# Kernel tuning notes

Measured on AMD Instinct MI355X. Metric: run time of the kernel, lower is better.

The kernel has to match this reference:

```python
import jax, jax.numpy as jnp
import numpy as np
from jax.ops import segment_sum, segment_min, segment_max

N, E = 25000, 400000
NF, EF = 30, 10
H = 40          # n_hidden (multiple of towers)
T = 5           # towers
F = H           # F_in per tower (divide_input=False)
FO = H // T     # F_out per tower
L = 2           # gnn layers
NC = 2          # classes
EPS_BN = 1e-5


def setup_inputs() -> dict:
    key = jax.random.key(0)
    ks = jax.random.split(key, 24)
    r = lambda k, s, sc=0.1: jax.random.normal(k, s, jnp.float32) * sc
    return {
        "x": jax.random.normal(ks[0], (N, NF), jnp.float32),
        "edge_attr": jax.random.normal(ks[1], (E, EF), jnp.float32),
        "edge_index": jax.random.randint(ks[2], (2, E), 0, N, jnp.int32),
        "node_w": r(ks[3], (NF, H)), "node_b": r(ks[4], (H,)),
        "edge_w": r(ks[5], (EF, H)), "edge_b": r(ks[6], (H,)),
        "enc_w": r(ks[7], (L, H, F)), "enc_b": r(ks[8], (L, F)),
        "pre_w": r(ks[9], (L, T, 3 * F, F)), "pre_b": r(ks[10], (L, T, F)),
        "post_w": r(ks[11], (L, T, 13 * F, FO)), "post_b": r(ks[12], (L, T, FO)),
        "lin_w": r(ks[13], (L, H, H)), "lin_b": r(ks[14], (L, H)),
        "bn_g": jnp.ones((L, H), jnp.float32), "bn_b": jnp.zeros((L, H), jnp.float32),
        "mlp1_w": r(ks[15], (3 * H, 50)), "mlp1_b": r(ks[16], (50,)),
        "mlp2_w": r(ks[17], (50, 25)), "mlp2_b": r(ks[18], (25,)),
        "mlp3_w": r(ks[19], (25, NC)), "mlp3_b": r(ks[20], (NC,)),
    }


def _pna_conv(x, src, dst, e_emb, enc_w, enc_b, pre_w, pre_b, post_w, post_b,
              lin_w, lin_b, cnt, cnt1, amp, att):
    # message: per-tower pre-MLP on cat(x_i=dst, x_j=src, enc(edge_attr))
    e = e_emb @ enc_w + enc_b                                    # [E, F]
    h = jnp.concatenate([x[dst], x[src], e], axis=-1)            # [E, 3F]
    hs = jnp.einsum('ef,tfo->eto', h, pre_w) + pre_b             # [E, T, F]
    # multi-aggregation over incoming edges (index = dst)
    c = cnt1[:, None, None]
    mean = segment_sum(hs, dst, num_segments=N) / c
    msq = segment_sum(hs * hs, dst, num_segments=N) / c
    std = jnp.sqrt(jax.nn.relu(msq - mean * mean) + 1e-5)
    has = (cnt > 0)[:, None, None]
    mn = jnp.where(has, segment_min(hs, dst, num_segments=N), 0.0)
    mx = jnp.where(has, segment_max(hs, dst, num_segments=N), 0.0)
    agg = jnp.concatenate([mean, mn, mx, std], axis=-1)          # [N, T, 4F]
    agg = jnp.concatenate([agg, agg * amp, agg * att], axis=-1)  # [N, T, 12F]
    out = jnp.concatenate(
        [jnp.broadcast_to(x[:, None, :], (N, T, F)), agg], axis=-1)  # [N, T, 13F]
    out = jnp.einsum('ntf,tfo->nto', out, post_w) + post_b       # [N, T, FO]
    return out.reshape(N, T * FO) @ lin_w + lin_b                # [N, H]


def reference(x, edge_attr, node_w, node_b, edge_w, edge_b, enc_w, enc_b,
              pre_w, pre_b, post_w, post_b, lin_w, lin_b, bn_g, bn_b,
              mlp1_w, mlp1_b, mlp2_w, mlp2_b, mlp3_w, mlp3_b, edge_index):
    src, dst = edge_index[0], edge_index[1]
    cnt = segment_sum(jnp.ones((E,), jnp.float32), dst, num_segments=N)  # in-degree
    cnt1 = jnp.maximum(cnt, 1.0)                                 # deg.clamp_(1)
    log_deg = jnp.log(cnt1 + 1.0)
    avg_log = jnp.mean(jnp.log(cnt + 1.0))                       # PNA avg_deg['log']
    amp = (log_deg / avg_log)[:, None, None]
    att = (avg_log / log_deg)[:, None, None]
    h = x @ node_w + node_b                                      # node embedding
    e_emb = edge_attr @ edge_w + edge_b                          # edge embedding
    for i in range(L):
        c = _pna_conv(h, src, dst, e_emb, enc_w[i], enc_b[i], pre_w[i], pre_b[i],
                      post_w[i], post_b[i], lin_w[i], lin_b[i], cnt, cnt1, amp, att)
        mu = jnp.mean(c, axis=0)
        var = jnp.mean((c - mu) ** 2, axis=0)                    # BatchNorm (batch stats)
        cbn = (c - mu) / jnp.sqrt(var + EPS_BN) * bn_g[i] + bn_b[i]
        h = (h + jax.nn.relu(cbn)) / 2.0
    z = jax.nn.relu(jnp.concatenate([h[src], h[dst]], axis=-1))  # [E, 2H]
    z = jnp.concatenate([z, e_emb], axis=-1)                     # [E, 3H]
    z = jax.nn.relu(z @ mlp1_w + mlp1_b)
    z = jax.nn.relu(z @ mlp2_w + mlp2_b)
    return z @ mlp3_w + mlp3_b                                   # [E, NC]
```

## Files before the change

### kernel.cpp

```cpp
#include <hip/hip_runtime.h>
#include <hip/hip_bf16.h>
#include <cstdint>
#include <cstddef>

#define NN 25000
#define NE 400000
#define NFD 30
#define EFD 10
#define H 40
#define T 5
#define FO 8
#define LAYERS 2
#define TF 200
#define BASE_W 800
#define PSTR 52
#define WS_PAD 532
#define REC 12
#define WCN 416
#define WCK 64
#define SHP 72
#define EPSV 1e-5f

typedef __attribute__((ext_vector_type(8))) short bf16x8;
typedef __attribute__((ext_vector_type(4))) float f32x4;

__device__ inline short bfbits(float v) {
    __hip_bfloat16 b = __float2bfloat16(v);
    return *(short*)&b;
}

__global__ __launch_bounds__(256) void k_deg(const int* __restrict__ dst, int* __restrict__ cnt) {
    int e = blockIdx.x * 256 + threadIdx.x;
    if (e < NE) atomicAdd(&cnt[dst[e]], 1);
}

__global__ __launch_bounds__(256) void k_avglog(const int* __restrict__ cnt, float* __restrict__ slot) {
    __shared__ float red[256];
    float s = 0.0f;
    for (int i = blockIdx.x * 256 + threadIdx.x; i < NN; i += gridDim.x * 256)
        s += logf((float)cnt[i] + 1.0f);
    red[threadIdx.x] = s; __syncthreads();
    for (int o = 128; o > 0; o >>= 1) {
        if (threadIdx.x < o) red[threadIdx.x] += red[threadIdx.x + o];
        __syncthreads();
    }
    if (threadIdx.x == 0) atomicAdd(slot, red[0]);
}

__global__ __launch_bounds__(256) void k_node(const float* __restrict__ x, const float* __restrict__ w,
                                              const float* __restrict__ b, float* __restrict__ h,
                                              const int* __restrict__ cnt, const float* __restrict__ slot,
                                              float* __restrict__ amp, float* __restrict__ att) {
    int id = blockIdx.x * 256 + threadIdx.x;
    if (id < NN) {
        float avg = slot[0] / (float)NN;
        float c1 = fmaxf((float)cnt[id], 1.0f);
        float lg = logf(c1 + 1.0f);
        amp[id] = lg / avg;
        att[id] = avg / lg;
    }
    if (id >= NN * H) return;
    int n = id / H, j = id - n * H;
    const float* xr = x + (size_t)n * NFD;
    float acc = b[j];
    #pragma unroll
    for (int m = 0; m < NFD; m++) acc += xr[m] * w[m * H + j];
    h[id] = acc;
}

__global__ __launch_bounds__(1024) void k_scan(const int* __restrict__ cnt, int* __restrict__ offs) {
    __shared__ int wsum[16];
    int tid = threadIdx.x;
    int lane = tid & 63, wv = tid >> 6;
    int runbase = 0;
    for (int base = 0; base < NN; base += 4096) {
        int i0 = base + tid * 4;
        int4 v = make_int4(0, 0, 0, 0);
        if (i0 < NN) v = *(const int4*)(cnt + i0);
        int tsum = v.x + v.y + v.z + v.w;
        int x = tsum;
        #pragma unroll
        for (int o = 1; o < 64; o <<= 1) {
            int y = __shfl_up(x, o);
            if (lane >= o) x += y;
        }
        if (lane == 63) wsum[wv] = x;
        __syncthreads();
        if (wv == 0 && lane < 16) {
            int wsv = wsum[lane];
            #pragma unroll
            for (int o = 1; o < 16; o <<= 1) {
                int y = __shfl_up(wsv, o);
                if (lane >= o) wsv += y;
            }
            wsum[lane] = wsv;
        }
        __syncthreads();
        int wpref = (wv > 0) ? wsum[wv - 1] : 0;
        int excl = runbase + wpref + x - tsum;
        if (i0 < NN) {
            offs[i0]     = excl;
            offs[i0 + 1] = excl + v.x;
            offs[i0 + 2] = excl + v.x + v.y;
            offs[i0 + 3] = excl + v.x + v.y + v.z;
        }
        runbase += wsum[15];
        __syncthreads();
    }
    if (tid == 0) offs[NN] = runbase;
}

__global__ __launch_bounds__(256) void k_scatter(const int* __restrict__ src, const int* __restrict__ dst,
                                                 const float* __restrict__ edge_attr,
                                                 const int* __restrict__ offs, int* __restrict__ fill,
                                                 float* __restrict__ ea_csr, int* __restrict__ pdst) {
    int e = blockIdx.x * 256 + threadIdx.x;
    if (e >= NE) return;
    int d = dst[e];
    int p = offs[d] + atomicAdd(&fill[d], 1);
    const float2* ear = (const float2*)(edge_attr + (size_t)e * EFD);
    float2 v0 = ear[0], v1 = ear[1], v2 = ear[2], v3 = ear[3], v4 = ear[4];
    float4* o = (float4*)(ea_csr + (size_t)p * REC);
    o[0] = make_float4(v0.x, v0.y, v1.x, v1.y);
    o[1] = make_float4(v2.x, v2.y, v3.x, v3.y);
    o[2] = make_float4(v4.x, v4.y, __int_as_float(src[e]), __int_as_float(e));
    pdst[p] = d;
}

__global__ __launch_bounds__(256) void k_prep1(const float* __restrict__ enc_w, const float* __restrict__ enc_b,
                                               const float* __restrict__ edge_w, const float* __restrict__ edge_b,
                                               const float* __restrict__ pre_w, const float* __restrict__ pre_b,
                                               const float* __restrict__ w1, const float* __restrict__ b1,
                                               float* __restrict__ W3e, float* __restrict__ dvecF,
                                               __hip_bfloat16* __restrict__ Wcat,
                                               float* __restrict__ W1e, float* __restrict__ b1e, int layer) {
    int id = blockIdx.x * 256 + threadIdx.x;
    if (id < EFD * TF) {
        int m = id / TF, j = id - m * TF;
        int t = j / H, f = j - t * H;
        const float* ew = enc_w + (size_t)layer * H * H;
        const float* pw = pre_w + (size_t)(layer * T + t) * 120 * H;
        float acc = 0.0f;
        for (int k = 0; k < H; k++) {
            float wk = edge_w[m * H + k];
            float g = 0.0f;
            #pragma unroll
            for (int o = 0; o < H; o++) g += ew[k * H + o] * pw[(80 + o) * H + f];
            acc += wk * g;
        }
        W3e[m * TF + j] = acc;
        if (m == 0) {
            const float* eb = enc_b + (size_t)layer * H;
            float dacc = pre_b[(size_t)(layer * T + t) * H + f];
            for (int o = 0; o < H; o++) {
                float ebe = eb[o];
                #pragma unroll
                for (int k = 0; k < H; k++) ebe += edge_b[k] * ew[k * H + o];
                dacc += ebe * pw[(80 + o) * H + f];
            }
            dvecF[j] = dacc;
        }
    } else if (id < EFD * TF + WCN * WCK) {
        int id2 = id - EFD * TF;
        int j = id2 / WCK, k = id2 - j * WCK;
        float val = 0.0f;
        if (k < H) {
            if (j < TF) {
                int t = j / H, f = j - t * H;
                val = pre_w[((size_t)(layer * T + t) * 120 + k) * H + f];
            } else if (j >= 208 && j < 208 + TF) {
                int j2 = j - 208;
                int t = j2 / H, f = j2 - t * H;
                val = pre_w[((size_t)(layer * T + t) * 120 + H + k) * H + f];
            }
        }
        Wcat[id2] = __float2bfloat16(val);
    } else if (layer == 0 && id < EFD * TF + WCN * WCK + EFD * 50) {
        int id2 = id - EFD * TF - WCN * WCK;
        int m = id2 / 50, o = id2 - m * 50;
        float acc = 0.0f;
        #pragma unroll
        for (int k = 0; k < H; k++) acc += edge_w[m * H + k] * w1[(80 + k) * 50 + o];
        W1e[m * 50 + o] = acc;
        if (m == 0) {
            float bacc = b1[o];
            #pragma unroll
            for (int k = 0; k < H; k++) bacc += edge_b[k] * w1[(80 + k) * 50 + o];
            b1e[o] = bacc;
        }
    }
}

__global__ __launch_bounds__(256) void k_abm(float* h, const float* __restrict__ cbuf,
                                             const float* __restrict__ bnsum, const float* __restrict__ bnsq,
                                             const float* __restrict__ bng, const float* __restrict__ bnb,
                                             int doBN,
                                             const __hip_bfloat16* __restrict__ Wcat,
                                             float* __restrict__ A, __hip_bfloat16* __restrict__ Bbf) {
    __shared__ short sh[64 * SHP];
    int tid = threadIdx.x;
    int n0 = blockIdx.x * 64;
    int nodes = NN - n0; if (nodes > 64) nodes = 64;
    for (int i = tid; i < 64 * SHP; i += 256) sh[i] = 0;
    __syncthreads();
    float invN = 1.0f / (float)NN;
    for (int i = tid; i < nodes * H; i += 256) {
        int f = i % H;
        float hv = h[(size_t)n0 * H + i];
        float hn;
        if (doBN) {
            float mu = bnsum[f] * invN;
            float var = bnsq[f] * invN - mu * mu;
            float c = (cbuf[(size_t)n0 * H + i] - mu) * rsqrtf(var + EPSV) * bng[f] + bnb[f];
            hn = (hv + fmaxf(c, 0.0f)) * 0.5f;
            h[(size_t)n0 * H + i] = hn;
        } else {
            hn = hv;
        }
        sh[(i / H) * SHP + f] = bfbits(hn);
    }
    __syncthreads();

    int wv = tid >> 6, lane = tid & 63;
    int q = lane >> 4, c16 = lane & 15;
    const short* arow = sh + (wv * 16 + c16) * SHP + q * 8;
    bf16x8 a0 = *(const bf16x8*)(arow);
    bf16x8 a1 = *(const bf16x8*)(arow + 32);
    int gm = n0 + wv * 16 + q * 4;

    for (int jt = 0; jt < 26; jt++) {
        int col = jt * 16 + c16;
        const short* wrow = (const short*)Wcat + (size_t)col * WCK + q * 8;
        bf16x8 b0 = *(const bf16x8*)(wrow);
        bf16x8 b1 = *(const bf16x8*)(wrow + 32);
        f32x4 acc = {0.0f, 0.0f, 0.0f, 0.0f};
        acc = __builtin_amdgcn_mfma_f32_16x16x32_bf16(a0, b0, acc, 0, 0, 0);
        acc = __builtin_amdgcn_mfma_f32_16x16x32_bf16(a1, b1, acc, 0, 0, 0);
        if (col < TF) {
            #pragma unroll
            for (int r = 0; r < 4; r++) {
                int row = gm + r;
                if (row < NN) A[(size_t)row * TF + col] = acc[r];
            }
        } else if (col >= 208) {
            int c2 = col - 208;
            if (c2 < TF) {
                #pragma unroll
                for (int r = 0; r < 4; r++) {
                    int row = gm + r;
                    if (row < NN) Bbf[(size_t)row * TF + c2] = __float2bfloat16(acc[r]);
                }
            }
        }
    }
}

__global__ __launch_bounds__(256) void k_agg(const float* __restrict__ ea_csr,
                                             const __hip_bfloat16* __restrict__ Bbf,
                                             const float* __restrict__ A, const float* __restrict__ w3e,
                                             const float* __restrict__ dvecF, const int* __restrict__ cnt,
                                             const int* __restrict__ offs, float* __restrict__ base) {
    int tid = threadIdx.x;
    int lane = tid & 63;
    int n = __builtin_amdgcn_readfirstlane((int)(blockIdx.x * 4 + (tid >> 6)));
    int deg = cnt[n];
    int start = offs[n];
    bool comp = lane < TF / 4;
    float4 w3q[EFD];
    float4 dj4 = make_float4(0, 0, 0, 0), a4 = make_float4(0, 0, 0, 0);
    if (comp) {
        #pragma unroll
        for (int m = 0; m < EFD; m++) w3q[m] = *(const float4*)(w3e + m * TF + 4 * lane);
        dj4 = *(const float4*)(dvecF + 4 * lane);
        a4  = *(const float4*)(A + (size_t)n * TF + 4 * lane);
    }
    float sx = 0, sy = 0, sz = 0, sw_ = 0;
    float qx = 0, qy = 0, qz = 0, qw = 0;
    float mnx = 3.4e38f, mny = 3.4e38f, mnz = 3.4e38f, mnw = 3.4e38f;
    float mxx = -3.4e38f, mxy = -3.4e38f, mxz = -3.4e38f, mxw = -3.4e38f;
    const float4* recb = (const float4*)ea_csr + (size_t)start * 3;
    const uint16_t* Bu = (const uint16_t*)Bbf;

    auto edge = [&](float4 qa, float4 qb, float4 qc, uint2 bv) {
        float b0 = __uint_as_float(bv.x << 16);
        float b1 = __uint_as_float(bv.x & 0xffff0000u);
        float b2 = __uint_as_float(bv.y << 16);
        float b3 = __uint_as_float(bv.y & 0xffff0000u);
        float eav[EFD] = {qa.x, qa.y, qa.z, qa.w, qb.x, qb.y, qb.z, qb.w, qc.x, qc.y};
        float cx = dj4.x, cy = dj4.y, cz = dj4.z, cw = dj4.w;
        #pragma unroll
        for (int m = 0; m < EFD; m++) {
            cx = fmaf(eav[m], w3q[m].x, cx);
            cy = fmaf(eav[m], w3q[m].y, cy);
            cz = fmaf(eav[m], w3q[m].z, cz);
            cw = fmaf(eav[m], w3q[m].w, cw);
        }
        float ux = b0 + cx, uy = b1 + cy, uz = b2 + cz, uw = b3 + cw;
        sx += ux; qx = fmaf(ux, ux, qx); mnx = fminf(mnx, ux); mxx = fmaxf(mxx, ux);
        sy += uy; qy = fmaf(uy, uy, qy); mny = fminf(mny, uy); mxy = fmaxf(mxy, uy);
        sz += uz; qz = fmaf(uz, uz, qz); mnz = fminf(mnz, uz); mxz = fmaxf(mxz, uz);
        sw_ += uw; qw = fmaf(uw, uw, qw); mnw = fminf(mnw, uw); mxw = fmaxf(mxw, uw);
    };

    int r = 0;
    for (; r + 4 <= deg; r += 4) {
        float4 qa0 = recb[(r + 0) * 3], qb0 = recb[(r + 0) * 3 + 1], qc0 = recb[(r + 0) * 3 + 2];
        float4 qa1 = recb[(r + 1) * 3], qb1 = recb[(r + 1) * 3 + 1], qc1 = recb[(r + 1) * 3 + 2];
        float4 qa2 = recb[(r + 2) * 3], qb2 = recb[(r + 2) * 3 + 1], qc2 = recb[(r + 2) * 3 + 2];
        float4 qa3 = recb[(r + 3) * 3], qb3 = recb[(r + 3) * 3 + 1], qc3 = recb[(r + 3) * 3 + 2];
        int s0 = __float_as_int(qc0.z), s1 = __float_as_int(qc1.z);
        int s2 = __float_as_int(qc2.z), s3 = __float_as_int(qc3.z);
        if (comp) {
            uint2 v0 = *(const uint2*)(Bu + (size_t)s0 * TF + 4 * lane);
            uint2 v1 = *(const uint2*)(Bu + (size_t)s1 * TF + 4 * lane);
            uint2 v2 = *(const uint2*)(Bu + (size_t)s2 * TF + 4 * lane);
            uint2 v3 = *(const uint2*)(Bu + (size_t)s3 * TF + 4 * lane);
            edge(qa0, qb0, qc0, v0);
            edge(qa1, qb1, qc1, v1);
            edge(qa2, qb2, qc2, v2);
            edge(qa3, qb3, qc3, v3);
        }
    }
    for (; r < deg; r++) {
        float4 qa = recb[r * 3], qb = recb[r * 3 + 1], qc = recb[r * 3 + 2];
        int sn = __float_as_int(qc.z);
        if (comp) {
            uint2 bv = *(const uint2*)(Bu + (size_t)sn * TF + 4 * lane);
            edge(qa, qb, qc, bv);
        }
    }
    if (comp) {
        float d = (float)deg, c1 = fmaxf(d, 1.0f);
        float inv = 1.0f / c1;
        float mex = (d * a4.x + sx) * inv, mey = (d * a4.y + sy) * inv;
        float mez = (d * a4.z + sz) * inv, mew = (d * a4.w + sw_) * inv;
        float msx = (d * a4.x * a4.x + 2.0f * a4.x * sx + qx) * inv;
        float msy = (d * a4.y * a4.y + 2.0f * a4.y * sy + qy) * inv;
        float msz = (d * a4.z * a4.z + 2.0f * a4.z * sz + qz) * inv;
        float msw = (d * a4.w * a4.w + 2.0f * a4.w * sw_ + qw) * inv;
        float4 mean4 = make_float4(mex, mey, mez, mew);
        float4 sd4 = make_float4(sqrtf(fmaxf(msx - mex * mex, 0.0f) + EPSV),
                                 sqrtf(fmaxf(msy - mey * mey, 0.0f) + EPSV),
                                 sqrtf(fmaxf(msz - mez * mez, 0.0f) + EPSV),
                                 sqrtf(fmaxf(msw - mew * mew, 0.0f) + EPSV));
        bool has = deg > 0;
        float4 mnv4 = has ? make_float4(a4.x + mnx, a4.y + mny, a4.z + mnz, a4.w + mnw)
                          : make_float4(0, 0, 0, 0);
        float4 mxv4 = has ? make_float4(a4.x + mxx, a4.y + mxy, a4.z + mxz, a4.w + mxw)
                          : make_float4(0, 0, 0, 0);
        int j0 = 4 * lane;
        int t = j0 / H, f = j0 - t * H;
        float* bb = base + (size_t)n * BASE_W + t * 160 + f;
        *(float4*)(bb)       = mean4;
        *(float4*)(bb + 40)  = mnv4;
        *(float4*)(bb + 80)  = mxv4;
        *(float4*)(bb + 120) = sd4;
    }
}

__global__ __launch_bounds__(256) void k_post(const float* __restrict__ h, const float* __restrict__ base,
                                              const float* __restrict__ amp, const float* __restrict__ att,
                                              const float* __restrict__ post_w, const float* __restrict__ post_b,
                                              float* __restrict__ cpre, int layer) {
    __shared__ float ws[FO * WS_PAD];
    int tid = threadIdx.x;
    int t = blockIdx.y;
    const float* pwsrc = post_w + (size_t)(layer * T + t) * 520 * FO;
    for (int i = tid; i < 520 * FO; i += 256) {
        int g = i >> 3, o = i & 7;
        ws[o * WS_PAD + g] = pwsrc[i];
    }
    __syncthreads();
    int slot = tid >> 3, o = tid & 7;
    int n0 = blockIdx.x * 64 + slot * 2;
    if (n0 >= NN) return;
    int n1 = n0 + 1;
    bool two = (n1 < NN);
    if (!two) n1 = n0;
    const float* wrow = ws + o * WS_PAD;
    float am0 = amp[n0], at0 = att[n0];
    float am1 = amp[n1], at1 = att[n1];
    float pb = post_b[(size_t)(layer * T + t) * FO + o];
    float acc0 = pb, acc1 = pb;
    const float4* hx0 = (const float4*)(h + (size_t)n0 * H);
    const float4* hx1 = (const float4*)(h + (size_t)n1 * H);
    #pragma unroll
    for (int g4 = 0; g4 < 10; g4++) {
        float4 wv = *(const float4*)(wrow + g4 * 4);
        float4 x0 = hx0[g4], x1 = hx1[g4];
        acc0 += x0.x * wv.x + x0.y * wv.y + x0.z * wv.z + x0.w * wv.w;
        acc1 += x1.x * wv.x + x1.y * wv.y + x1.z * wv.z + x1.w * wv.w;
    }
    const float4* b0 = (const float4*)(base + (size_t)n0 * BASE_W + t * 160);
    const float4* b1 = (const float4*)(base + (size_t)n1 * BASE_W + t * 160);
    #pragma unroll 8
    for (int g4 = 0; g4 < 40; g4++) {
        float4 wa = *(const float4*)(wrow + 40 + g4 * 4);
        float4 wb = *(const float4*)(wrow + 200 + g4 * 4);
        float4 wc = *(const float4*)(wrow + 360 + g4 * 4);
        float4 v0 = b0[g4], v1 = b1[g4];
        acc0 += v0.x * (wa.x + am0 * wb.x + at0 * wc.x)
              + v0.y * (wa.y + am0 * wb.y + at0 * wc.y)
              + v0.z * (wa.z + am0 * wb.z + at0 * wc.z)
              + v0.w * (wa.w + am0 * wb.w + at0 * wc.w);
        acc1 += v1.x * (wa.x + am1 * wb.x + at1 * wc.x)
              + v1.y * (wa.y + am1 * wb.y + at1 * wc.y)
              + v1.z * (wa.z + am1 * wb.z + at1 * wc.z)
              + v1.w * (wa.w + am1 * wb.w + at1 * wc.w);
    }
    cpre[(size_t)n0 * H + t * FO + o] = acc0;
    if (two) cpre[(size_t)n1 * H + t * FO + o] = acc1;
}

__global__ __launch_bounds__(256) void k_linbn(const float* __restrict__ cpre, const float* __restrict__ lin_w,
                                               const float* __restrict__ lin_b, float* __restrict__ cbuf,
                                               float* __restrict__ bnsum, float* __restrict__ bnsq, int layer) {
    __shared__ float scp[240];
    __shared__ float red[80];
    int tid = threadIdx.x;
    int j = tid % H, nl = tid / H;
    const float* lw = lin_w + (size_t)layer * H * H;
    float wcol[H];
    #pragma unroll
    for (int k = 0; k < H; k++) wcol[k] = lw[k * H + j];
    float lb = lin_b[(size_t)layer * H + j];
    float lsum = 0.0f, lsq = 0.0f;
    for (int n0 = blockIdx.x * 6; n0 < NN; n0 += gridDim.x * 6) {
        int nn = NN - n0; if (nn > 6) nn = 6;
        if (tid < nn * H) scp[tid] = cpre[(size_t)n0 * H + tid];
        __syncthreads();
        if (nl < nn) {
            float acc = lb;
            #pragma unroll
            for (int k = 0; k < H; k++) acc += scp[nl * H + k] * wcol[k];
            cbuf[(size_t)(n0 + nl) * H + j] = acc;
            lsum += acc; lsq += acc * acc;
        }
        __syncthreads();
    }
    if (tid < 80) red[tid] = 0.0f;
    __syncthreads();
    if (nl < 6) { atomicAdd(&red[j], lsum); atomicAdd(&red[40 + j], lsq); }
    __syncthreads();
    if (tid < 40) atomicAdd(&bnsum[tid], red[tid]);
    else if (tid < 80) atomicAdd(&bnsq[tid - 40], red[tid]);
}

__global__ __launch_bounds__(256) void k_prep2(const float* __restrict__ h, const float* __restrict__ cbuf,
                                               const float* __restrict__ bnsum, const float* __restrict__ bnsq,
                                               const float* __restrict__ bng, const float* __restrict__ bnb,
                                               const float* __restrict__ w1,
                                               float* __restrict__ P1, float* __restrict__ P2) {
    __shared__ float sh[5 * H];
    int tid = threadIdx.x;
    int n0 = blockIdx.x * 5;
    if (tid < 5 * H) {
        int j = tid % H;
        float invN = 1.0f / (float)NN;
        float mu = bnsum[j] * invN;
        float var = bnsq[j] * invN - mu * mu;
        float inv = rsqrtf(var + EPSV);
        float cv = (cbuf[(size_t)n0 * H + tid] - mu) * inv * bng[j] + bnb[j];
        sh[tid] = (h[(size_t)n0 * H + tid] + fmaxf(cv, 0.0f)) * 0.5f;
    }
    __syncthreads();
    if (tid >= 250) return;
    int nl = tid / 50, o = tid - nl * 50;
    const float* hr = sh + nl * H;
    float a1 = 0.0f, a2 = 0.0f;
    #pragma unroll
    for (int f = 0; f < H; f++) {
        float v = fmaxf(hr[f], 0.0f);
        a1 += v * w1[f * 50 + o];
        a2 += v * w1[(H + f) * 50 + o];
    }
    P1[(size_t)(n0 + nl) * PSTR + o] = a1;
    P2[(size_t)(n0 + nl) * PSTR + o] = a2;
}

__global__ __launch_bounds__(256) void k_mlp(const float* __restrict__ ea_csr, const int* __restrict__ pdst,
                                             const float* __restrict__ P1, const float* __restrict__ P2,
                                             const float* __restrict__ W1e, const float* __restrict__ b1e,
                                             const float* __restrict__ w2, const float* __restrict__ b2,
                                             const float* __restrict__ w3, const float* __restrict__ b3,
                                             float* __restrict__ out) {
    int p = blockIdx.x * 256 + threadIdx.x;
    if (p >= NE) return;
    const float4* rec = (const float4*)ea_csr + (size_t)p * 3;
    float4 r0 = rec[0], r1 = rec[1], r2 = rec[2];
    int s = __float_as_int(r2.z), eid = __float_as_int(r2.w);
    int d = pdst[p];
    float ea[EFD] = {r0.x, r0.y, r0.z, r0.w, r1.x, r1.y, r1.z, r1.w, r2.x, r2.y};

    float z1[52];
    const float4* p1r = (const float4*)(P1 + (size_t)s * PSTR);
    const float4* p2r = (const float4*)(P2 + (size_t)d * PSTR);
    #pragma unroll
    for (int i = 0; i < 13; i++) {
        float4 a = p1r[i], b = p2r[i];
        z1[4 * i]     = a.x + b.x;
        z1[4 * i + 1] = a.y + b.y;
        z1[4 * i + 2] = a.z + b.z;
        z1[4 * i + 3] = a.w + b.w;
    }
    #pragma unroll
    for (int k = 0; k < 50; k++) z1[k] += b1e[k];
    #pragma unroll
    for (int m = 0; m < EFD; m++) {
        float v = ea[m];
        #pragma unroll
        for (int k = 0; k < 50; k++) z1[k] = fmaf(v, W1e[m * 50 + k], z1[k]);
    }
    float z2[25];
    #pragma unroll
    for (int o = 0; o < 25; o++) z2[o] = b2[o];
    #pragma unroll
    for (int k = 0; k < 50; k++) {
        float v = fmaxf(z1[k], 0.0f);
        #pragma unroll
        for (int o = 0; o < 25; o++) z2[o] = fmaf(v, w2[k * 25 + o], z2[o]);
    }
    float o0 = b3[0], o1 = b3[1];
    #pragma unroll
    for (int k = 0; k < 25; k++) {
        float v = fmaxf(z2[k], 0.0f);
        o0 = fmaf(v, w3[k * 2], o0);
        o1 = fmaf(v, w3[k * 2 + 1], o1);
    }
    *(float2*)(out + (size_t)eid * 2) = make_float2(o0, o1);
}

extern "C" void kernel_launch(void* const* d_in, const int* in_sizes, int n_in,
                              void* d_out, int out_size, void* d_ws, size_t ws_size,
                              hipStream_t stream) {
    const float* x         = (const float*)d_in[0];
    const float* edge_attr = (const float*)d_in[1];
    const int*   eidx      = (const int*)  d_in[2];
    const float* node_w    = (const float*)d_in[3];
    const float* node_b    = (const float*)d_in[4];
    const float* edge_w    = (const float*)d_in[5];
    const float* edge_b    = (const float*)d_in[6];
    const float* enc_w     = (const float*)d_in[7];
    const float* enc_b     = (const float*)d_in[8];
    const float* pre_w     = (const float*)d_in[9];
    const float* pre_b     = (const float*)d_in[10];
    const float* post_w    = (const float*)d_in[11];
    const float* post_b    = (const float*)d_in[12];
    const float* lin_w     = (const float*)d_in[13];
    const float* lin_b     = (const float*)d_in[14];
    const float* bn_g      = (const float*)d_in[15];
    const float* bn_b      = (const float*)d_in[16];
    const float* w1 = (const float*)d_in[17];
    const float* b1 = (const float*)d_in[18];
    const float* w2 = (const float*)d_in[19];
    const float* b2 = (const float*)d_in[20];
    const float* w3 = (const float*)d_in[21];
    const float* b3 = (const float*)d_in[22];
    const int* srcp = eidx;
    const int* dstp = eidx + NE;
    float* out = (float*)d_out;

    char* ws = (char*)d_ws;
    size_t off = 0;
    auto alloc = [&](size_t bytes) -> char* {
        char* p = ws + off;
        off += (bytes + 255) & ~(size_t)255;
        return p;
    };
    float* h      = (float*)alloc((size_t)NN * H * 4);
    float* Abuf   = (float*)alloc((size_t)NN * TF * 4);
    float* cbuf   = (float*)alloc((size_t)NN * H * 4);
    __hip_bfloat16* Bbf = (__hip_bfloat16*)alloc((size_t)NN * TF * 2 + 256);
    float* base   = (float*)alloc((size_t)NN * BASE_W * 4);
    float* cpre   = (float*)alloc((size_t)NN * H * 4);
    float* ea_csr = (float*)alloc((size_t)NE * REC * 4);
    int* pdst     = (int*)alloc((size_t)NE * 4);
    float* W3e    = (float*)alloc((size_t)EFD * TF * 4);
    float* dvecF  = (float*)alloc((size_t)TF * 4);
    __hip_bfloat16* Wcat = (__hip_bfloat16*)alloc((size_t)WCN * WCK * 2);
    float* P1     = (float*)alloc((size_t)NN * PSTR * 4);
    float* P2     = (float*)alloc((size_t)NN * PSTR * 4);
    float* W1e    = (float*)alloc((size_t)EFD * 50 * 4);
    float* b1e    = (float*)alloc((size_t)64 * 4);
    float* amp    = (float*)alloc((size_t)NN * 4);
    float* att    = (float*)alloc((size_t)NN * 4);
    int* offs     = (int*)alloc((size_t)(NN + 1) * 4);
    size_t zoff = off;
    int* cnt_i    = (int*)alloc((size_t)NN * 4);
    int* fill     = (int*)alloc((size_t)NN * 4);
    float* avgs   = (float*)alloc(256);
    float* bnz    = (float*)alloc(1024);
    size_t zsize = off - zoff;
    if (off > ws_size) return;

    hipMemsetAsync(cnt_i, 0, zsize, stream);

    k_deg<<<(NE + 255) / 256, 256, 0, stream>>>(dstp, cnt_i);
    k_avglog<<<64, 256, 0, stream>>>(cnt_i, avgs);
    k_node<<<(NN * H + 255) / 256, 256, 0, stream>>>(x, node_w, node_b, h, cnt_i, avgs, amp, att);
    k_scan<<<1, 1024, 0, stream>>>(cnt_i, offs);
    k_scatter<<<(NE + 255) / 256, 256, 0, stream>>>(srcp, dstp, edge_attr, offs, fill, ea_csr, pdst);

    int prep1_grid = (EFD * TF + WCN * WCK + EFD * 50 + 255) / 256;
    for (int layer = 0; layer < LAYERS; layer++) {
        float* bnzL = bnz + layer * 128;
        k_prep1<<<prep1_grid, 256, 0, stream>>>(
            enc_w, enc_b, edge_w, edge_b, pre_w, pre_b, w1, b1,
            W3e, dvecF, Wcat, W1e, b1e, layer);
        float* bnzP = bnz + (layer - 1) * 128;
        k_abm<<<(NN + 63) / 64, 256, 0, stream>>>(
            h, cbuf, (layer > 0) ? bnzP : bnz, (layer > 0) ? bnzP + 40 : bnz,
            bn_g + (size_t)(layer > 0 ? layer - 1 : 0) * H,
            bn_b + (size_t)(layer > 0 ? layer - 1 : 0) * H,
            (layer > 0) ? 1 : 0, Wcat, Abuf, Bbf);
        k_agg<<<NN / 4, 256, 0, stream>>>(ea_csr, Bbf, Abuf, W3e, dvecF, cnt_i, offs, base);
        k_post<<<dim3((NN + 63) / 64, T), 256, 0, stream>>>(h, base, amp, att, post_w, post_b, cpre, layer);
        k_linbn<<<1024, 256, 0, stream>>>(cpre, lin_w, lin_b, cbuf, bnzL, bnzL + 40, layer);
    }
    k_prep2<<<NN / 5, 256, 0, stream>>>(h, cbuf, bnz + 128, bnz + 168,
                                        bn_g + H, bn_b + H, w1, P1, P2);
    k_mlp<<<(NE + 255) / 256, 256, 0, stream>>>(ea_csr, pdst, P1, P2, W1e, b1e, w2, b2, w3, b3, out);
}
```

Measured before the change: 587.5 us.

## Fuse post-aggregation tower MLP into aggregation kernel via shared memory

Removes the separate post kernel and the 800-float-per-node base buffer. The aggregation kernel now stages each block's four nodes' aggregates in shared memory and applies the per-tower post weights there: amplification and attenuation scalars are applied to partial dot products, and the h-term is added via a reordered Wxd matrix prepared in prep1. This removes the global write and read of roughly 80 MB per layer, at the cost of extra LDS (about 16 KB), two block syncs and more work per aggregation block, which may reduce occupancy.

```diff
diff --git a/kernel.cpp b/kernel.cpp
--- a/kernel.cpp
+++ b/kernel.cpp
@@ -12,9 +12,7 @@
 #define FO 8
 #define LAYERS 2
 #define TF 200
-#define BASE_W 800
 #define PSTR 52
-#define WS_PAD 532
 #define REC 12
 #define WCN 416
 #define WCK 64
@@ -130,12 +128,19 @@
 __global__ __launch_bounds__(256) void k_prep1(const float* __restrict__ enc_w, const float* __restrict__ enc_b,
                                                const float* __restrict__ edge_w, const float* __restrict__ edge_b,
                                                const float* __restrict__ pre_w, const float* __restrict__ pre_b,
+                                               const float* __restrict__ post_w,
                                                const float* __restrict__ w1, const float* __restrict__ b1,
                                                float* __restrict__ W3e, float* __restrict__ dvecF,
                                                __hip_bfloat16* __restrict__ Wcat,
+                                               float* __restrict__ Wp, float* __restrict__ Wxd,
                                                float* __restrict__ W1e, float* __restrict__ b1e, int layer) {
     int id = blockIdx.x * 256 + threadIdx.x;
-    if (id < EFD * TF) {
+    const int B0 = EFD * TF;
+    const int B1 = B0 + WCN * WCK;
+    const int B2 = B1 + EFD * 50;
+    const int B3 = B2 + 120 * 160;
+    const int B4 = B3 + H * H;
+    if (id < B0) {
         int m = id / TF, j = id - m * TF;
         int t = j / H, f = j - t * H;
         const float* ew = enc_w + (size_t)layer * H * H;
@@ -160,8 +165,8 @@
             }
             dvecF[j] = dacc;
         }
-    } else if (id < EFD * TF + WCN * WCK) {
-        int id2 = id - EFD * TF;
+    } else if (id < B1) {
+        int id2 = id - B0;
         int j = id2 / WCK, k = id2 - j * WCK;
         float val = 0.0f;
         if (k < H) {
@@ -175,19 +180,32 @@
             }
         }
         Wcat[id2] = __float2bfloat16(val);
-    } else if (layer == 0 && id < EFD * TF + WCN * WCK + EFD * 50) {
-        int id2 = id - EFD * TF - WCN * WCK;
-        int m = id2 / 50, o = id2 - m * 50;
-        float acc = 0.0f;
-        #pragma unroll
-        for (int k = 0; k < H; k++) acc += edge_w[m * H + k] * w1[(80 + k) * 50 + o];
-        W1e[m * 50 + o] = acc;
-        if (m == 0) {
-            float bacc = b1[o];
+    } else if (id < B2) {
+        if (layer == 0) {
+            int id2 = id - B1;
+            int m = id2 / 50, o = id2 - m * 50;
+            float acc = 0.0f;
             #pragma unroll
-            for (int k = 0; k < H; k++) bacc += edge_b[k] * w1[(80 + k) * 50 + o];
-            b1e[o] = bacc;
-        }
+            for (int k = 0; k < H; k++) acc += edge_w[m * H + k] * w1[(80 + k) * 50 + o];
+            W1e[m * 50 + o] = acc;
+            if (m == 0) {
+                float bacc = b1[o];
+                #pragma unroll
+                for (int k = 0; k < H; k++) bacc += edge_b[k] * w1[(80 + k) * 50 + o];
+                b1e[o] = bacc;
+            }
+        }
+    } else if (id < B3) {
+        int i2 = id - B2;
+        int col = i2 / 160, fs = i2 - col * 160;
+        int t = col / 24, rem = col - t * 24;
+        int grp = rem >> 3, o = rem & 7;
+        Wp[i2] = post_w[((size_t)(layer * T + t) * 520 + 40 + grp * 160 + fs) * FO + o];
+    } else if (id < B4) {
+        int i2 = id - B3;
+        int j = i2 / H, f = i2 - j * H;
+        int t = j >> 3, o = j & 7;
+        Wxd[i2] = post_w[((size_t)(layer * T + t) * 520 + f) * FO + o];
     }
 }
 
@@ -259,10 +277,21 @@
                                              const __hip_bfloat16* __restrict__ Bbf,
                                              const float* __restrict__ A, const float* __restrict__ w3e,
                                              const float* __restrict__ dvecF, const int* __restrict__ cnt,
-                                             const int* __restrict__ offs, float* __restrict__ base) {
+                                             const int* __restrict__ offs,
+                                             const float* __restrict__ h,
+                                             const float* __restrict__ Wp, const float* __restrict__ Wxd,
+                                             const float* __restrict__ pbL,
+                                             const float* __restrict__ amp, const float* __restrict__ att,
+                                             float* __restrict__ cpre) {
+    __shared__ float sst[4 * 800];
+    __shared__ float spart[4 * 120 * 2];
+    __shared__ float shh[4 * H];
     int tid = threadIdx.x;
     int lane = tid & 63;
-    int n = __builtin_amdgcn_readfirstlane((int)(blockIdx.x * 4 + (tid >> 6)));
+    int wv = tid >> 6;
+    int n0 = blockIdx.x * 4;
+    int n = __builtin_amdgcn_readfirstlane((int)(n0 + wv));
+    if (tid < 4 * H) shh[tid] = h[(size_t)n0 * H + tid];
     int deg = cnt[n];
     int start = offs[n];
     bool comp = lane < TF / 4;
@@ -350,66 +379,59 @@
                           : make_float4(0, 0, 0, 0);
         int j0 = 4 * lane;
         int t = j0 / H, f = j0 - t * H;
-        float* bb = base + (size_t)n * BASE_W + t * 160 + f;
-        *(float4*)(bb)       = mean4;
-        *(float4*)(bb + 40)  = mnv4;
-        *(float4*)(bb + 80)  = mxv4;
-        *(float4*)(bb + 120) = sd4;
-    }
-}
-
-__global__ __launch_bounds__(256) void k_post(const float* __restrict__ h, const float* __restrict__ base,
-                                              const float* __restrict__ amp, const float* __restrict__ att,
-                                              const float* __restrict__ post_w, const float* __restrict__ post_b,
-                                              float* __restrict__ cpre, int layer) {
-    __shared__ float ws[FO * WS_PAD];
-    int tid = threadIdx.x;
-    int t = blockIdx.y;
-    const float* pwsrc = post_w + (size_t)(layer * T + t) * 520 * FO;
-    for (int i = tid; i < 520 * FO; i += 256) {
-        int g = i >> 3, o = i & 7;
-        ws[o * WS_PAD + g] = pwsrc[i];
+        float* sb = sst + wv * 800 + t * 160 + f;
+        *(float4*)(sb)       = mean4;
+        *(float4*)(sb + 40)  = mnv4;
+        *(float4*)(sb + 80)  = mxv4;
+        *(float4*)(sb + 120) = sd4;
     }
     __syncthreads();
-    int slot = tid >> 3, o = tid & 7;
-    int n0 = blockIdx.x * 64 + slot * 2;
-    if (n0 >= NN) return;
-    int n1 = n0 + 1;
-    bool two = (n1 < NN);
-    if (!two) n1 = n0;
-    const float* wrow = ws + o * WS_PAD;
-    float am0 = amp[n0], at0 = att[n0];
-    float am1 = amp[n1], at1 = att[n1];
-    float pb = post_b[(size_t)(layer * T + t) * FO + o];
-    float acc0 = pb, acc1 = pb;
-    const float4* hx0 = (const float4*)(h + (size_t)n0 * H);
-    const float4* hx1 = (const float4*)(h + (size_t)n1 * H);
-    #pragma unroll
-    for (int g4 = 0; g4 < 10; g4++) {
-        float4 wv = *(const float4*)(wrow + g4 * 4);
-        float4 x0 = hx0[g4], x1 = hx1[g4];
-        acc0 += x0.x * wv.x + x0.y * wv.y + x0.z * wv.z + x0.w * wv.w;
-        acc1 += x1.x * wv.x + x1.y * wv.y + x1.z * wv.z + x1.w * wv.w;
-    }
-    const float4* b0 = (const float4*)(base + (size_t)n0 * BASE_W + t * 160);
-    const float4* b1 = (const float4*)(base + (size_t)n1 * BASE_W + t * 160);
-    #pragma unroll 8
-    for (int g4 = 0; g4 < 40; g4++) {
-        float4 wa = *(const float4*)(wrow + 40 + g4 * 4);
-        float4 wb = *(const float4*)(wrow + 200 + g4 * 4);
-        float4 wc = *(const float4*)(wrow + 360 + g4 * 4);
-        float4 v0 = b0[g4], v1 = b1[g4];
-        acc0 += v0.x * (wa.x + am0 * wb.x + at0 * wc.x)
-              + v0.y * (wa.y + am0 * wb.y + at0 * wc.y)
-              + v0.z * (wa.z + am0 * wb.z + at0 * wc.z)
-              + v0.w * (wa.w + am0 * wb.w + at0 * wc.w);
-        acc1 += v1.x * (wa.x + am1 * wb.x + at1 * wc.x)
-              + v1.y * (wa.y + am1 * wb.y + at1 * wc.y)
-              + v1.z * (wa.z + am1 * wb.z + at1 * wc.z)
-              + v1.w * (wa.w + am1 * wb.w + at1 * wc.w);
-    }
-    cpre[(size_t)n0 * H + t * FO + o] = acc0;
-    if (two) cpre[(size_t)n1 * H + t * FO + o] = acc1;
+
+    if (tid < 240) {
+        int out = tid >> 1, half = tid & 1;
+        int t = out / 24;
+        const float* wrow = Wp + (size_t)out * 160 + half * 80;
+        const float* sb0 = sst + t * 160 + half * 80;
+        float a0 = 0.f, a1 = 0.f, a2 = 0.f, a3 = 0.f;
+        #pragma unroll
+        for (int q = 0; q < 20; q++) {
+            float4 w = *(const float4*)(wrow + q * 4);
+            float4 v0 = *(const float4*)(sb0 + q * 4);
+            float4 v1 = *(const float4*)(sb0 + 800 + q * 4);
+            float4 v2 = *(const float4*)(sb0 + 1600 + q * 4);
+            float4 v3 = *(const float4*)(sb0 + 2400 + q * 4);
+            a0 += v0.x * w.x + v0.y * w.y + v0.z * w.z + v0.w * w.w;
+            a1 += v1.x * w.x + v1.y * w.y + v1.z * w.z + v1.w * w.w;
+            a2 += v2.x * w.x + v2.y * w.y + v2.z * w.z + v2.w * w.w;
+            a3 += v3.x * w.x + v3.y * w.y + v3.z * w.z + v3.w * w.w;
+        }
+        spart[(0 * 120 + out) * 2 + half] = a0;
+        spart[(1 * 120 + out) * 2 + half] = a1;
+        spart[(2 * 120 + out) * 2 + half] = a2;
+        spart[(3 * 120 + out) * 2 + half] = a3;
+    }
+    __syncthreads();
+
+    if (tid < 160) {
+        int nd = tid / H, j = tid - nd * H;
+        int t = j >> 3, o = j & 7;
+        int ng = n0 + nd;
+        float am = amp[ng], at = att[ng];
+        const float* sp = spart + (nd * 120 + t * 24) * 2;
+        float pa = sp[o * 2]            + sp[o * 2 + 1];
+        float pb = sp[(8 + o) * 2]      + sp[(8 + o) * 2 + 1];
+        float pc = sp[(16 + o) * 2]     + sp[(16 + o) * 2 + 1];
+        float acc = pbL[j] + pa + am * pb + at * pc;
+        const float* hr = shh + nd * H;
+        const float* wx = Wxd + (size_t)j * H;
+        #pragma unroll
+        for (int fq = 0; fq < 10; fq++) {
+            float4 hv = *(const float4*)(hr + fq * 4);
+            float4 wv = *(const float4*)(wx + fq * 4);
+            acc += hv.x * wv.x + hv.y * wv.y + hv.z * wv.z + hv.w * wv.w;
+        }
+        cpre[(size_t)ng * H + j] = acc;
+    }
 }
 
 __global__ __launch_bounds__(256) void k_linbn(const float* __restrict__ cpre, const float* __restrict__ lin_w,
@@ -571,13 +593,14 @@
     float* Abuf   = (float*)alloc((size_t)NN * TF * 4);
     float* cbuf   = (float*)alloc((size_t)NN * H * 4);
     __hip_bfloat16* Bbf = (__hip_bfloat16*)alloc((size_t)NN * TF * 2 + 256);
-    float* base   = (float*)alloc((size_t)NN * BASE_W * 4);
     float* cpre   = (float*)alloc((size_t)NN * H * 4);
     float* ea_csr = (float*)alloc((size_t)NE * REC * 4);
     int* pdst     = (int*)alloc((size_t)NE * 4);
     float* W3e    = (float*)alloc((size_t)EFD * TF * 4);
     float* dvecF  = (float*)alloc((size_t)TF * 4);
     __hip_bfloat16* Wcat = (__hip_bfloat16*)alloc((size_t)WCN * WCK * 2);
+    float* Wp     = (float*)alloc((size_t)120 * 160 * 4);
+    float* Wxd    = (float*)alloc((size_t)H * H * 4);
     float* P1     = (float*)alloc((size_t)NN * PSTR * 4);
     float* P2     = (float*)alloc((size_t)NN * PSTR * 4);
     float* W1e    = (float*)alloc((size_t)EFD * 50 * 4);
@@ -601,20 +624,22 @@
     k_scan<<<1, 1024, 0, stream>>>(cnt_i, offs);
     k_scatter<<<(NE + 255) / 256, 256, 0, stream>>>(srcp, dstp, edge_attr, offs, fill, ea_csr, pdst);
 
-    int prep1_grid = (EFD * TF + WCN * WCK + EFD * 50 + 255) / 256;
+    int prep1_tot = EFD * TF + WCN * WCK + EFD * 50 + 120 * 160 + H * H;
+    int prep1_grid = (prep1_tot + 255) / 256;
     for (int layer = 0; layer < LAYERS; layer++) {
         float* bnzL = bnz + layer * 128;
         k_prep1<<<prep1_grid, 256, 0, stream>>>(
-            enc_w, enc_b, edge_w, edge_b, pre_w, pre_b, w1, b1,
-            W3e, dvecF, Wcat, W1e, b1e, layer);
+            enc_w, enc_b, edge_w, edge_b, pre_w, pre_b, post_w, w1, b1,
+            W3e, dvecF, Wcat, Wp, Wxd, W1e, b1e, layer);
         float* bnzP = bnz + (layer - 1) * 128;
         k_abm<<<(NN + 63) / 64, 256, 0, stream>>>(
             h, cbuf, (layer > 0) ? bnzP : bnz, (layer > 0) ? bnzP + 40 : bnz,
             bn_g + (size_t)(layer > 0 ? layer - 1 : 0) * H,
             bn_b + (size_t)(layer > 0 ? layer - 1 : 0) * H,
             (layer > 0) ? 1 : 0, Wcat, Abuf, Bbf);
-        k_agg<<<NN / 4, 256, 0, stream>>>(ea_csr, Bbf, Abuf, W3e, dvecF, cnt_i, offs, base);
-        k_post<<<dim3((NN + 63) / 64, T), 256, 0, stream>>>(h, base, amp, att, post_w, post_b, cpre, layer);
+        k_agg<<<NN / 4, 256, 0, stream>>>(ea_csr, Bbf, Abuf, W3e, dvecF, cnt_i, offs,
+                                          h, Wp, Wxd, post_b + (size_t)layer * T * FO,
+                                          amp, att, cpre);
         k_linbn<<<1024, 256, 0, stream>>>(cpre, lin_w, lin_b, cbuf, bnzL, bnzL + 40, layer);
     }
     k_prep2<<<NN / 5, 256, 0, stream>>>(h, cbuf, bnz + 128, bnz + 168,
```

Measured after the change: 612.8 us. 1.04x slower.
